# Performance work log

Measured on AMD Instinct MI355X. Metric: run time of the kernel, lower is better.

The kernel has to match this reference:

```python
import jax, jax.numpy as jnp
import numpy as np

N_NODES = 50000
N_EDGES = 1600000
N_GRAPHS = 64
F_IN = 256
H = 1024
EPS = 1e-5


def setup_inputs() -> dict:
    key = jax.random.key(0)
    ks = jax.random.split(key, 6)
    x = jax.random.normal(ks[0], (N_NODES, F_IN), dtype=jnp.float32)
    edge_index = jax.random.randint(ks[1], (2, N_EDGES), 0, N_NODES, dtype=jnp.int32)
    batch = jnp.sort(jax.random.randint(ks[2], (N_NODES,), 0, N_GRAPHS, dtype=jnp.int32))
    # Glorot-ish init for GCN weights
    W0 = jax.random.normal(ks[3], (F_IN, H), dtype=jnp.float32) * (1.0 / np.sqrt(F_IN))
    b0 = jnp.zeros((H,), dtype=jnp.float32)
    Ws = jax.random.normal(ks[4], (3, H, H), dtype=jnp.float32) * (1.0 / np.sqrt(H))
    bs = jnp.zeros((3, H), dtype=jnp.float32)
    gammas = jnp.ones((4, H), dtype=jnp.float32)
    betas = jnp.zeros((4, H), dtype=jnp.float32)
    return {"x": x, "edge_index": edge_index, "batch": batch,
            "W0": W0, "b0": b0, "Ws": Ws, "bs": bs,
            "gammas": gammas, "betas": betas}


def _gcn_norm(edge_index, n_nodes):
    # Add self-loops (PyG GCNConv default), compute symmetric normalization.
    loops = jnp.arange(n_nodes, dtype=edge_index.dtype)
    row = jnp.concatenate([edge_index[0], loops])  # sources
    col = jnp.concatenate([edge_index[1], loops])  # targets (aggregation index)
    ones = jnp.ones(row.shape[0], dtype=jnp.float32)
    deg = jax.ops.segment_sum(ones, col, num_segments=n_nodes)
    dinv = jnp.where(deg > 0, jax.lax.rsqrt(deg), 0.0)
    norm = dinv[row] * dinv[col]  # [E + N]
    return row, col, norm


def _layer(h, W, b, gamma, beta, row, col, norm):
    ht = h @ W                                           # [N, H] GEMM
    msg = ht[row] * norm[:, None]                        # gather + scale
    agg = jax.ops.segment_sum(msg, col, num_segments=N_NODES) + b
    mu = jnp.mean(agg, axis=-1, keepdims=True)
    var = jnp.mean(jnp.square(agg - mu), axis=-1, keepdims=True)
    hn = (agg - mu) * jax.lax.rsqrt(var + EPS) * gamma + beta
    return jax.nn.relu(hn)


def reference(x, edge_index, batch, W0, b0, Ws, bs, gammas, betas):
    row, col, norm = _gcn_norm(edge_index, N_NODES)
    h = _layer(x, W0, b0, gammas[0], betas[0], row, col, norm)
    for i in range(3):
        h = _layer(h, Ws[i], bs[i], gammas[i + 1], betas[i + 1], row, col, norm)
    # scatter_mean over batch (graph-level pooling)
    sums = jax.ops.segment_sum(h, batch, num_segments=N_GRAPHS)
    cnt = jax.ops.segment_sum(jnp.ones((N_NODES,), jnp.float32), batch, num_segments=N_GRAPHS)
    return sums / jnp.maximum(cnt, 1.0)[:, None]
```

## Files before the change

kernel.cpp:

```cpp
#include <hip/hip_runtime.h>
#include <hip/hip_bf16.h>
#include <stdint.h>

#define NN 50000
#define NE 1600000
#define NG 64
#define FIN 256
#define HD 1024
#define EPSV 1e-5f

typedef __bf16 bf16;
typedef __bf16 bf16x4 __attribute__((ext_vector_type(4)));
typedef __bf16 bf16x8 __attribute__((ext_vector_type(8)));
typedef float f32x4 __attribute__((ext_vector_type(4)));

typedef const __attribute__((address_space(1))) void* gptr_as1;
typedef __attribute__((address_space(3))) void* lptr_as3;

__device__ __forceinline__ void load_g2l_16(const void* g, const void* l) {
  __builtin_amdgcn_global_load_lds((gptr_as1)(uintptr_t)g,
                                   (lptr_as3)(uint32_t)(uintptr_t)l, 16, 0, 0);
}

__global__ void hist_kernel(const int* __restrict__ col, int* __restrict__ cnt, int E) {
  int e = blockIdx.x * 256 + threadIdx.x;
  if (e < E) atomicAdd(&cnt[col[e]], 1);
}

__global__ void dinv_kernel(const int* __restrict__ cnt, float* __restrict__ dinv, int n) {
  int i = blockIdx.x * 256 + threadIdx.x;
  if (i < n) dinv[i] = rsqrtf((float)(cnt[i] + 1));
}

__global__ void scan_partial_kernel(const int* __restrict__ cnt, int* __restrict__ partial, int n) {
  __shared__ int red[4];
  int i = blockIdx.x * 256 + threadIdx.x;
  int v = (i < n) ? cnt[i] : 0;
  #pragma unroll
  for (int off = 32; off; off >>= 1) v += __shfl_down(v, off, 64);
  if ((threadIdx.x & 63) == 0) red[threadIdx.x >> 6] = v;
  __syncthreads();
  if (threadIdx.x == 0) partial[blockIdx.x] = red[0] + red[1] + red[2] + red[3];
}

__global__ void scan_scan_kernel(int* __restrict__ partial, int nb) {
  __shared__ int s[256];
  int t = threadIdx.x;
  int v = (t < nb) ? partial[t] : 0;
  s[t] = v;
  __syncthreads();
  for (int off = 1; off < 256; off <<= 1) {
    int x = (t >= off) ? s[t - off] : 0;
    __syncthreads();
    s[t] += x;
    __syncthreads();
  }
  if (t < nb) partial[t] = s[t] - v;
}

__global__ void scan_final_kernel(const int* __restrict__ cnt, const int* __restrict__ partial,
                                  int* __restrict__ row_ptr, int n, int E) {
  __shared__ int s[256];
  int t = threadIdx.x;
  int i = blockIdx.x * 256 + t;
  int v = (i < n) ? cnt[i] : 0;
  s[t] = v;
  __syncthreads();
  for (int off = 1; off < 256; off <<= 1) {
    int x = (t >= off) ? s[t - off] : 0;
    __syncthreads();
    s[t] += x;
    __syncthreads();
  }
  if (i < n) row_ptr[i] = partial[blockIdx.x] + s[t] - v;
  if (i == 0) row_ptr[n] = E;
}

__global__ void scatter_kernel(const int* __restrict__ rowi, const int* __restrict__ coli,
                               const int* __restrict__ row_ptr, int* __restrict__ fill,
                               const float* __restrict__ dinv,
                               int* __restrict__ csr_src, float* __restrict__ csr_w, int E) {
  int e = blockIdx.x * 256 + threadIdx.x;
  if (e >= E) return;
  int s = rowi[e], d = coli[e];
  int pos = row_ptr[d] + atomicAdd(&fill[d], 1);
  csr_src[pos] = s;
  csr_w[pos] = dinv[s] * dinv[d];
}

__global__ void cvt_kernel(const float* __restrict__ in, bf16* __restrict__ out, int n4) {
  int i = blockIdx.x * 256 + threadIdx.x;
  if (i >= n4) return;
  float4 v = ((const float4*)in)[i];
  bf16x4 o = { (bf16)v.x, (bf16)v.y, (bf16)v.z, (bf16)v.w };
  ((bf16x4*)out)[i] = o;
}

__global__ void transpose_w_kernel(const float* __restrict__ W, bf16* __restrict__ Wt,
                                   int K, int N) {
  __shared__ float tile[32][33];
  int n0 = blockIdx.x * 32, k0 = blockIdx.y * 32;
  int tx = threadIdx.x, ty = threadIdx.y;
  #pragma unroll
  for (int i = ty; i < 32; i += 8) tile[i][tx] = W[(size_t)(k0 + i) * N + n0 + tx];
  __syncthreads();
  #pragma unroll
  for (int i = ty; i < 32; i += 8) Wt[(size_t)(n0 + i) * K + k0 + tx] = (bf16)tile[tx][i];
}

__global__ __launch_bounds__(256, 2) void gemm_bt_kernel(
    const bf16* __restrict__ A, const bf16* __restrict__ Bt,
    bf16* __restrict__ C, int M, int K) {
  __shared__ __align__(16) bf16 As[2][128 * 32];
  __shared__ __align__(16) bf16 Bs[2][128 * 32];
  const int tid = threadIdx.x;
  const int w = tid >> 6, l = tid & 63;

  const int nwg = gridDim.x;
  const int o = blockIdx.x;
  const int lid = (o & 7) * (nwg >> 3) + (o >> 3);
  const int m0 = (lid >> 3) * 128, n0 = (lid & 7) * 128;
  const int wr = w >> 1, wc = w & 1;

  f32x4 acc[4][4] = {};

  const int r0 = tid >> 2;
  const int c8 = (tid & 3) * 8;
  int ar0 = m0 + r0;       if (ar0 >= M) ar0 = M - 1;
  int ar1 = m0 + r0 + 64;  if (ar1 >= M) ar1 = M - 1;
  const bf16* a0 = A + (size_t)ar0 * K + c8;
  const bf16* a1 = A + (size_t)ar1 * K + c8;
  const bf16* b0 = Bt + (size_t)(n0 + r0) * K + c8;
  const bf16* b1 = Bt + (size_t)(n0 + r0 + 64) * K + c8;

  const int mrow = l & 15;
  const int kch = (l >> 4) * 8;

  auto stage = [&](int b, int k) {
    bf16* asw = &As[b][w * 512];
    bf16* bsw = &Bs[b][w * 512];
    load_g2l_16(a0 + k, asw);
    load_g2l_16(a1 + k, asw + 2048);
    load_g2l_16(b0 + k, bsw);
    load_g2l_16(b1 + k, bsw + 2048);
  };

  const int nit = K >> 5;
  stage(0, 0);
  __syncthreads();

  int cur = 0;
  for (int t = 0; t < nit; ++t) {
    if (t + 1 < nit) stage(cur ^ 1, (t + 1) << 5);
    bf16x8 af[4], bf_[4];
    #pragma unroll
    for (int m = 0; m < 4; m++)
      af[m] = *(const bf16x8*)&As[cur][(wr * 64 + m * 16 + mrow) * 32 + kch];
    #pragma unroll
    for (int n = 0; n < 4; n++)
      bf_[n] = *(const bf16x8*)&Bs[cur][(wc * 64 + n * 16 + mrow) * 32 + kch];
    #pragma unroll
    for (int m = 0; m < 4; m++)
      #pragma unroll
      for (int n = 0; n < 4; n++)
        acc[m][n] = __builtin_amdgcn_mfma_f32_16x16x32_bf16(af[m], bf_[n], acc[m][n], 0, 0, 0);
    __syncthreads();
    cur ^= 1;
  }

  #pragma unroll
  for (int m = 0; m < 4; m++) {
    int grow = m0 + wr * 64 + m * 16 + (l >> 4) * 4;
    #pragma unroll
    for (int n = 0; n < 4; n++) {
      int gcol = n0 + wc * 64 + n * 16 + (l & 15);
      #pragma unroll
      for (int r = 0; r < 4; r++) {
        if (grow + r < M) C[(size_t)(grow + r) * HD + gcol] = (bf16)acc[m][n][r];
      }
    }
  }
}

__global__ __launch_bounds__(256) void quant_kernel(
    const bf16* __restrict__ ht, uint8_t* __restrict__ htu8, float* __restrict__ rowscale) {
  const int row = blockIdx.x;
  const int t = threadIdx.x;
  __shared__ float red[4];
  bf16x4 v = ((const bf16x4*)(ht + (size_t)row * HD))[t];
  float f0 = (float)v[0], f1 = (float)v[1], f2 = (float)v[2], f3 = (float)v[3];
  float m = fmaxf(fmaxf(fabsf(f0), fabsf(f1)), fmaxf(fabsf(f2), fabsf(f3)));
  #pragma unroll
  for (int off = 32; off; off >>= 1) m = fmaxf(m, __shfl_xor(m, off, 64));
  if ((t & 63) == 0) red[t >> 6] = m;
  __syncthreads();
  m = fmaxf(fmaxf(red[0], red[1]), fmaxf(red[2], red[3]));
  float inv = (m > 0.f) ? 127.0f / m : 0.f;
  int q0 = __float2int_rn(f0 * inv) + 128, q1 = __float2int_rn(f1 * inv) + 128;
  int q2 = __float2int_rn(f2 * inv) + 128, q3 = __float2int_rn(f3 * inv) + 128;
  uint32_t packed = ((uint32_t)(q0 & 0xff)) | ((uint32_t)(q1 & 0xff) << 8) |
                    ((uint32_t)(q2 & 0xff) << 16) | ((uint32_t)(q3 & 0xff) << 24);
  ((uint32_t*)htu8)[row * 256 + t] = packed;
  if (t == 0) rowscale[row] = (m > 0.f) ? m / 127.0f : 0.f;
}

__device__ __forceinline__ void acc_u8(float acc[8], float& sw, float w, uint2 d) {
  sw += w;
  acc[0] += w * (float)(d.x & 0xffu);
  acc[1] += w * (float)((d.x >> 8) & 0xffu);
  acc[2] += w * (float)((d.x >> 16) & 0xffu);
  acc[3] += w * (float)(d.x >> 24);
  acc[4] += w * (float)(d.y & 0xffu);
  acc[5] += w * (float)((d.y >> 8) & 0xffu);
  acc[6] += w * (float)((d.y >> 16) & 0xffu);
  acc[7] += w * (float)(d.y >> 24);
}

__global__ __launch_bounds__(256) void agg_ln_u8_kernel(
    const uint8_t* __restrict__ htu8, const float* __restrict__ rowscale,
    const int* __restrict__ row_ptr,
    const int* __restrict__ csr_src, const float* __restrict__ csr_w,
    const float* __restrict__ dinv, const float* __restrict__ bias,
    const float* __restrict__ gamma, const float* __restrict__ beta,
    bf16* __restrict__ hout) {
  const int g = threadIdx.x >> 7;
  const int node = blockIdx.x * 2 + g;
  const int tt = threadIdx.x & 127;
  const int wid = threadIdx.x >> 6;
  __shared__ float red[4];

  float acc[8] = {};
  float sw = 0.f;

  float dn = dinv[node];
  float wself = dn * dn * rowscale[node];
  acc_u8(acc, sw, wself, ((const uint2*)(htu8 + (size_t)node * HD))[tt]);

  int e = row_ptr[node];
  const int e1 = row_ptr[node + 1];
  for (; e + 4 <= e1; e += 4) {
    int s0 = csr_src[e], s1 = csr_src[e + 1], s2 = csr_src[e + 2], s3 = csr_src[e + 3];
    float w0 = csr_w[e] * rowscale[s0];
    float w1 = csr_w[e + 1] * rowscale[s1];
    float w2 = csr_w[e + 2] * rowscale[s2];
    float w3 = csr_w[e + 3] * rowscale[s3];
    uint2 d0 = ((const uint2*)(htu8 + (size_t)s0 * HD))[tt];
    uint2 d1 = ((const uint2*)(htu8 + (size_t)s1 * HD))[tt];
    uint2 d2 = ((const uint2*)(htu8 + (size_t)s2 * HD))[tt];
    uint2 d3 = ((const uint2*)(htu8 + (size_t)s3 * HD))[tt];
    acc_u8(acc, sw, w0, d0);
    acc_u8(acc, sw, w1, d1);
    acc_u8(acc, sw, w2, d2);
    acc_u8(acc, sw, w3, d3);
  }
  for (; e < e1; e++) {
    int src = csr_src[e];
    float wgt = csr_w[e] * rowscale[src];
    acc_u8(acc, sw, wgt, ((const uint2*)(htu8 + (size_t)src * HD))[tt]);
  }

  const float4* bias2 = (const float4*)bias;
  float4 ba = bias2[tt * 2], bb = bias2[tt * 2 + 1];
  float c128 = 128.0f * sw;
  acc[0] += ba.x - c128; acc[1] += ba.y - c128; acc[2] += ba.z - c128; acc[3] += ba.w - c128;
  acc[4] += bb.x - c128; acc[5] += bb.y - c128; acc[6] += bb.z - c128; acc[7] += bb.w - c128;

  float s = 0.f;
  #pragma unroll
  for (int j = 0; j < 8; j++) s += acc[j];
  #pragma unroll
  for (int off = 32; off; off >>= 1) s += __shfl_down(s, off, 64);
  if ((threadIdx.x & 63) == 0) red[wid] = s;
  __syncthreads();
  float mean = (red[g * 2] + red[g * 2 + 1]) * (1.0f / HD);
  __syncthreads();

  float d[8], s2 = 0.f;
  #pragma unroll
  for (int j = 0; j < 8; j++) { d[j] = acc[j] - mean; s2 += d[j] * d[j]; }
  #pragma unroll
  for (int off = 32; off; off >>= 1) s2 += __shfl_down(s2, off, 64);
  if ((threadIdx.x & 63) == 0) red[wid] = s2;
  __syncthreads();
  float var = (red[g * 2] + red[g * 2 + 1]) * (1.0f / HD);
  float rstd = rsqrtf(var + EPSV);

  const float4* gam2 = (const float4*)gamma;
  const float4* bet2 = (const float4*)beta;
  float4 g0 = gam2[tt * 2], g1 = gam2[tt * 2 + 1];
  float4 be0 = bet2[tt * 2], be1 = bet2[tt * 2 + 1];
  float gv[8] = {g0.x, g0.y, g0.z, g0.w, g1.x, g1.y, g1.z, g1.w};
  float bv[8] = {be0.x, be0.y, be0.z, be0.w, be1.x, be1.y, be1.z, be1.w};
  bf16x8 o;
  #pragma unroll
  for (int j = 0; j < 8; j++) o[j] = (bf16)fmaxf(d[j] * rstd * gv[j] + bv[j], 0.0f);
  ((bf16x8*)(hout + (size_t)node * HD))[tt] = o;
}

__global__ void starts_kernel(const int* __restrict__ batch, int* __restrict__ start,
                              int n, int ngraph) {
  int g = blockIdx.x * blockDim.x + threadIdx.x;
  if (g > ngraph) return;
  int lo = 0, hi = n;
  while (lo < hi) {
    int mid = (lo + hi) >> 1;
    if (batch[mid] < g) lo = mid + 1; else hi = mid;
  }
  start[g] = lo;
}

#define POOL_CHUNKS 8
__global__ void pool_partial_kernel(const bf16* __restrict__ h, const int* __restrict__ start,
                                    float* __restrict__ out) {
  int g = blockIdx.y, c = blockIdx.x;
  int t = threadIdx.x;
  int s0 = start[g], s1 = start[g + 1];
  int len = s1 - s0;
  int per = (len + POOL_CHUNKS - 1) / POOL_CHUNKS;
  int a = s0 + c * per;
  int b = min(a + per, s1);
  if (a >= b) return;
  f32x4 acc = {0.f, 0.f, 0.f, 0.f};
  for (int n = a; n < b; n++) {
    bf16x4 v = ((const bf16x4*)(h + (size_t)n * HD))[t];
    acc[0] += (float)v[0]; acc[1] += (float)v[1];
    acc[2] += (float)v[2]; acc[3] += (float)v[3];
  }
  float* o = out + (size_t)g * HD + t * 4;
  atomicAdd(o + 0, acc[0]);
  atomicAdd(o + 1, acc[1]);
  atomicAdd(o + 2, acc[2]);
  atomicAdd(o + 3, acc[3]);
}

__global__ void pool_div_kernel(float* __restrict__ out, const int* __restrict__ start) {
  int i = blockIdx.x * 256 + threadIdx.x;
  if (i >= NG * HD) return;
  int g = i >> 10;
  float c = (float)max(start[g + 1] - start[g], 1);
  out[i] = out[i] / c;
}

extern "C" void kernel_launch(void* const* d_in, const int* in_sizes, int n_in,
                              void* d_out, int out_size, void* d_ws, size_t ws_size,
                              hipStream_t stream) {
  const float* x      = (const float*)d_in[0];
  const int*   eidx   = (const int*)d_in[1];
  const int*   batch  = (const int*)d_in[2];
  const float* W0     = (const float*)d_in[3];
  const float* b0     = (const float*)d_in[4];
  const float* Ws     = (const float*)d_in[5];
  const float* bs     = (const float*)d_in[6];
  const float* gammas = (const float*)d_in[7];
  const float* betas  = (const float*)d_in[8];
  float* out = (float*)d_out;

  const int* erow = eidx;
  const int* ecol = eidx + NE;

  char* ws = (char*)d_ws;
  size_t off = 0;
  auto alloc = [&](size_t bytes) {
    void* p = ws + off;
    off = (off + bytes + 255) & ~(size_t)255;
    return p;
  };
  int*   cnt     = (int*)alloc((size_t)NN * 4);
  int*   row_ptr = (int*)alloc((size_t)(NN + 1) * 4);
  int*   fill    = (int*)alloc((size_t)NN * 4);
  int*   partial = (int*)alloc(256 * 4);
  float* dinv    = (float*)alloc((size_t)NN * 4);
  int*   csr_src = (int*)alloc((size_t)NE * 4);
  float* csr_w   = (float*)alloc((size_t)NE * 4);
  bf16*  Wt      = (bf16*)alloc((size_t)HD * HD * 2);
  bf16*  hbuf    = (bf16*)alloc((size_t)NN * HD * 2);
  bf16*  htbuf   = (bf16*)alloc((size_t)NN * HD * 2);
  int*   gstart  = (int*)alloc(65 * 4);
  float* rowscale = (float*)cnt;

  hipMemsetAsync(cnt, 0, (size_t)NN * 4, stream);
  hipMemsetAsync(fill, 0, (size_t)NN * 4, stream);
  hipMemsetAsync(out, 0, (size_t)NG * HD * 4, stream);

  hist_kernel<<<(NE + 255) / 256, 256, 0, stream>>>(ecol, cnt, NE);
  dinv_kernel<<<(NN + 255) / 256, 256, 0, stream>>>(cnt, dinv, NN);
  int nb = (NN + 255) / 256;
  scan_partial_kernel<<<nb, 256, 0, stream>>>(cnt, partial, NN);
  scan_scan_kernel<<<1, 256, 0, stream>>>(partial, nb);
  scan_final_kernel<<<nb, 256, 0, stream>>>(cnt, partial, row_ptr, NN, NE);
  scatter_kernel<<<(NE + 255) / 256, 256, 0, stream>>>(erow, ecol, row_ptr, fill, dinv,
                                                       csr_src, csr_w, NE);
  starts_kernel<<<1, 128, 0, stream>>>(batch, gstart, NN, NG);

  bf16* A = hbuf;
  bf16* B = htbuf;

  cvt_kernel<<<(NN * FIN / 4 + 255) / 256, 256, 0, stream>>>(x, A, NN * FIN / 4);

  const int nmt = (NN + 127) / 128;
  for (int L = 0; L < 4; L++) {
    int K = (L == 0) ? FIN : HD;
    const float* W    = (L == 0) ? W0 : Ws + (size_t)(L - 1) * HD * HD;
    const float* bias = (L == 0) ? b0 : bs + (size_t)(L - 1) * HD;
    transpose_w_kernel<<<dim3(HD / 32, K / 32), dim3(32, 8), 0, stream>>>(W, Wt, K, HD);
    gemm_bt_kernel<<<nmt * 8, 256, 0, stream>>>(A, Wt, B, NN, K);
    quant_kernel<<<NN, 256, 0, stream>>>(B, (uint8_t*)A, rowscale);
    agg_ln_u8_kernel<<<NN / 2, 256, 0, stream>>>((const uint8_t*)A, rowscale, row_ptr,
                                                 csr_src, csr_w, dinv, bias,
                                                 gammas + (size_t)L * HD,
                                                 betas + (size_t)L * HD, B);
    bf16* tmp = A; A = B; B = tmp;
  }

  pool_partial_kernel<<<dim3(POOL_CHUNKS, NG), 256, 0, stream>>>(A, gstart, out);
  pool_div_kernel<<<(NG * HD + 255) / 256, 256, 0, stream>>>(out, gstart);
}
```

Before: 1.749 ms.

## Fuse int8 quantization into GEMM epilogue with per-128-column block scales

The GEMM epilogue now computes a per-row absmax over each 128-column tile and writes uint8 values plus a per-(row, column-block) scale straight to global memory. This removes the separate quant kernel and the bf16 round-trip of the full activation matrix. The aggregation kernel indexes the scale per column block instead of per row. In exchange there is extra shuffle and LDS work in the epilogue, byte-wise scattered stores, and more scale loads per edge during the gather.

```diff
diff --git a/kernel.cpp b/kernel.cpp
--- a/kernel.cpp
+++ b/kernel.cpp
@@ -108,11 +108,12 @@
   for (int i = ty; i < 32; i += 8) Wt[(size_t)(n0 + i) * K + k0 + tx] = (bf16)tile[tx][i];
 }
 
-__global__ __launch_bounds__(256, 2) void gemm_bt_kernel(
+__global__ __launch_bounds__(256, 2) void gemm_bt_q8_kernel(
     const bf16* __restrict__ A, const bf16* __restrict__ Bt,
-    bf16* __restrict__ C, int M, int K) {
+    uint8_t* __restrict__ C8, float* __restrict__ scales, int M, int K) {
   __shared__ __align__(16) bf16 As[2][128 * 32];
   __shared__ __align__(16) bf16 Bs[2][128 * 32];
+  __shared__ float smax[2][128];
   const int tid = threadIdx.x;
   const int w = tid >> 6, l = tid & 63;
 
@@ -120,6 +121,7 @@
   const int o = blockIdx.x;
   const int lid = (o & 7) * (nwg >> 3) + (o >> 3);
   const int m0 = (lid >> 3) * 128, n0 = (lid & 7) * 128;
+  const int cb = lid & 7;
   const int wr = w >> 1, wc = w & 1;
 
   f32x4 acc[4][4] = {};
@@ -168,40 +170,47 @@
     cur ^= 1;
   }
 
+  float pmax[4][4];
+  #pragma unroll
+  for (int m = 0; m < 4; m++)
+    #pragma unroll
+    for (int r = 0; r < 4; r++) {
+      float v = 0.f;
+      #pragma unroll
+      for (int n = 0; n < 4; n++) v = fmaxf(v, fabsf(acc[m][n][r]));
+      #pragma unroll
+      for (int mask = 1; mask < 16; mask <<= 1) v = fmaxf(v, __shfl_xor(v, mask, 64));
+      pmax[m][r] = v;
+    }
+  if ((l & 15) == 0) {
+    #pragma unroll
+    for (int m = 0; m < 4; m++)
+      #pragma unroll
+      for (int r = 0; r < 4; r++)
+        smax[wc][wr * 64 + m * 16 + (l >> 4) * 4 + r] = pmax[m][r];
+  }
+  __syncthreads();
+
   #pragma unroll
   for (int m = 0; m < 4; m++) {
-    int grow = m0 + wr * 64 + m * 16 + (l >> 4) * 4;
-    #pragma unroll
-    for (int n = 0; n < 4; n++) {
-      int gcol = n0 + wc * 64 + n * 16 + (l & 15);
-      #pragma unroll
-      for (int r = 0; r < 4; r++) {
-        if (grow + r < M) C[(size_t)(grow + r) * HD + gcol] = (bf16)acc[m][n][r];
+    #pragma unroll
+    for (int r = 0; r < 4; r++) {
+      int rl = wr * 64 + m * 16 + (l >> 4) * 4 + r;
+      int grow = m0 + rl;
+      float mx = fmaxf(smax[0][rl], smax[1][rl]);
+      float inv = (mx > 0.f) ? 127.0f / mx : 0.f;
+      if (grow < M) {
+        if (wc == 0 && (l & 15) == 0)
+          scales[(size_t)grow * 8 + cb] = (mx > 0.f) ? mx / 127.0f : 0.f;
+        #pragma unroll
+        for (int n = 0; n < 4; n++) {
+          int gcol = n0 + wc * 64 + n * 16 + (l & 15);
+          int u = __float2int_rn(acc[m][n][r] * inv) + 128;
+          C8[(size_t)grow * HD + gcol] = (uint8_t)u;
+        }
       }
     }
   }
-}
-
-__global__ __launch_bounds__(256) void quant_kernel(
-    const bf16* __restrict__ ht, uint8_t* __restrict__ htu8, float* __restrict__ rowscale) {
-  const int row = blockIdx.x;
-  const int t = threadIdx.x;
-  __shared__ float red[4];
-  bf16x4 v = ((const bf16x4*)(ht + (size_t)row * HD))[t];
-  float f0 = (float)v[0], f1 = (float)v[1], f2 = (float)v[2], f3 = (float)v[3];
-  float m = fmaxf(fmaxf(fabsf(f0), fabsf(f1)), fmaxf(fabsf(f2), fabsf(f3)));
-  #pragma unroll
-  for (int off = 32; off; off >>= 1) m = fmaxf(m, __shfl_xor(m, off, 64));
-  if ((t & 63) == 0) red[t >> 6] = m;
-  __syncthreads();
-  m = fmaxf(fmaxf(red[0], red[1]), fmaxf(red[2], red[3]));
-  float inv = (m > 0.f) ? 127.0f / m : 0.f;
-  int q0 = __float2int_rn(f0 * inv) + 128, q1 = __float2int_rn(f1 * inv) + 128;
-  int q2 = __float2int_rn(f2 * inv) + 128, q3 = __float2int_rn(f3 * inv) + 128;
-  uint32_t packed = ((uint32_t)(q0 & 0xff)) | ((uint32_t)(q1 & 0xff) << 8) |
-                    ((uint32_t)(q2 & 0xff) << 16) | ((uint32_t)(q3 & 0xff) << 24);
-  ((uint32_t*)htu8)[row * 256 + t] = packed;
-  if (t == 0) rowscale[row] = (m > 0.f) ? m / 127.0f : 0.f;
 }
 
 __device__ __forceinline__ void acc_u8(float acc[8], float& sw, float w, uint2 d) {
@@ -217,7 +226,7 @@
 }
 
 __global__ __launch_bounds__(256) void agg_ln_u8_kernel(
-    const uint8_t* __restrict__ htu8, const float* __restrict__ rowscale,
+    const uint8_t* __restrict__ htu8, const float* __restrict__ scales,
     const int* __restrict__ row_ptr,
     const int* __restrict__ csr_src, const float* __restrict__ csr_w,
     const float* __restrict__ dinv, const float* __restrict__ bias,
@@ -226,6 +235,7 @@
   const int g = threadIdx.x >> 7;
   const int node = blockIdx.x * 2 + g;
   const int tt = threadIdx.x & 127;
+  const int cbL = tt >> 4;
   const int wid = threadIdx.x >> 6;
   __shared__ float red[4];
 
@@ -233,17 +243,17 @@
   float sw = 0.f;
 
   float dn = dinv[node];
-  float wself = dn * dn * rowscale[node];
+  float wself = dn * dn * scales[(size_t)node * 8 + cbL];
   acc_u8(acc, sw, wself, ((const uint2*)(htu8 + (size_t)node * HD))[tt]);
 
   int e = row_ptr[node];
   const int e1 = row_ptr[node + 1];
   for (; e + 4 <= e1; e += 4) {
     int s0 = csr_src[e], s1 = csr_src[e + 1], s2 = csr_src[e + 2], s3 = csr_src[e + 3];
-    float w0 = csr_w[e] * rowscale[s0];
-    float w1 = csr_w[e + 1] * rowscale[s1];
-    float w2 = csr_w[e + 2] * rowscale[s2];
-    float w3 = csr_w[e + 3] * rowscale[s3];
+    float w0 = csr_w[e] * scales[(size_t)s0 * 8 + cbL];
+    float w1 = csr_w[e + 1] * scales[(size_t)s1 * 8 + cbL];
+    float w2 = csr_w[e + 2] * scales[(size_t)s2 * 8 + cbL];
+    float w3 = csr_w[e + 3] * scales[(size_t)s3 * 8 + cbL];
     uint2 d0 = ((const uint2*)(htu8 + (size_t)s0 * HD))[tt];
     uint2 d1 = ((const uint2*)(htu8 + (size_t)s1 * HD))[tt];
     uint2 d2 = ((const uint2*)(htu8 + (size_t)s2 * HD))[tt];
@@ -255,7 +265,7 @@
   }
   for (; e < e1; e++) {
     int src = csr_src[e];
-    float wgt = csr_w[e] * rowscale[src];
+    float wgt = csr_w[e] * scales[(size_t)src * 8 + cbL];
     acc_u8(acc, sw, wgt, ((const uint2*)(htu8 + (size_t)src * HD))[tt]);
   }
 
@@ -365,18 +375,18 @@
     off = (off + bytes + 255) & ~(size_t)255;
     return p;
   };
-  int*   cnt     = (int*)alloc((size_t)NN * 4);
-  int*   row_ptr = (int*)alloc((size_t)(NN + 1) * 4);
-  int*   fill    = (int*)alloc((size_t)NN * 4);
-  int*   partial = (int*)alloc(256 * 4);
-  float* dinv    = (float*)alloc((size_t)NN * 4);
-  int*   csr_src = (int*)alloc((size_t)NE * 4);
-  float* csr_w   = (float*)alloc((size_t)NE * 4);
-  bf16*  Wt      = (bf16*)alloc((size_t)HD * HD * 2);
-  bf16*  hbuf    = (bf16*)alloc((size_t)NN * HD * 2);
-  bf16*  htbuf   = (bf16*)alloc((size_t)NN * HD * 2);
-  int*   gstart  = (int*)alloc(65 * 4);
-  float* rowscale = (float*)cnt;
+  int*     cnt     = (int*)alloc((size_t)NN * 4);
+  int*     row_ptr = (int*)alloc((size_t)(NN + 1) * 4);
+  int*     fill    = (int*)alloc((size_t)NN * 4);
+  int*     partial = (int*)alloc(256 * 4);
+  float*   dinv    = (float*)alloc((size_t)NN * 4);
+  int*     csr_src = (int*)alloc((size_t)NE * 4);
+  float*   csr_w   = (float*)alloc((size_t)NE * 4);
+  bf16*    Wt      = (bf16*)alloc((size_t)HD * HD * 2);
+  bf16*    hbuf    = (bf16*)alloc((size_t)NN * HD * 2);
+  uint8_t* ht8     = (uint8_t*)alloc((size_t)NN * HD);
+  float*   scales  = (float*)alloc((size_t)NN * 8 * 4);
+  int*     gstart  = (int*)alloc(65 * 4);
 
   hipMemsetAsync(cnt, 0, (size_t)NN * 4, stream);
   hipMemsetAsync(fill, 0, (size_t)NN * 4, stream);
@@ -392,10 +402,7 @@
                                                        csr_src, csr_w, NE);
   starts_kernel<<<1, 128, 0, stream>>>(batch, gstart, NN, NG);
 
-  bf16* A = hbuf;
-  bf16* B = htbuf;
-
-  cvt_kernel<<<(NN * FIN / 4 + 255) / 256, 256, 0, stream>>>(x, A, NN * FIN / 4);
+  cvt_kernel<<<(NN * FIN / 4 + 255) / 256, 256, 0, stream>>>(x, hbuf, NN * FIN / 4);
 
   const int nmt = (NN + 127) / 128;
   for (int L = 0; L < 4; L++) {
@@ -403,15 +410,12 @@
     const float* W    = (L == 0) ? W0 : Ws + (size_t)(L - 1) * HD * HD;
     const float* bias = (L == 0) ? b0 : bs + (size_t)(L - 1) * HD;
     transpose_w_kernel<<<dim3(HD / 32, K / 32), dim3(32, 8), 0, stream>>>(W, Wt, K, HD);
-    gemm_bt_kernel<<<nmt * 8, 256, 0, stream>>>(A, Wt, B, NN, K);
-    quant_kernel<<<NN, 256, 0, stream>>>(B, (uint8_t*)A, rowscale);
-    agg_ln_u8_kernel<<<NN / 2, 256, 0, stream>>>((const uint8_t*)A, rowscale, row_ptr,
-                                                 csr_src, csr_w, dinv, bias,
-                                                 gammas + (size_t)L * HD,
-                                                 betas + (size_t)L * HD, B);
-    bf16* tmp = A; A = B; B = tmp;
-  }
-
-  pool_partial_kernel<<<dim3(POOL_CHUNKS, NG), 256, 0, stream>>>(A, gstart, out);
+    gemm_bt_q8_kernel<<<nmt * 8, 256, 0, stream>>>(hbuf, Wt, ht8, scales, NN, K);
+    agg_ln_u8_kernel<<<NN / 2, 256, 0, stream>>>(ht8, scales, row_ptr, csr_src, csr_w,
+                                                 dinv, bias, gammas + (size_t)L * HD,
+                                                 betas + (size_t)L * HD, hbuf);
+  }
+
+  pool_partial_kernel<<<dim3(POOL_CHUNKS, NG), 256, 0, stream>>>(hbuf, gstart, out);
   pool_div_kernel<<<(NG * HD + 255) / 256, 256, 0, stream>>>(out, gstart);
 }
```

Result: faster. 1.681 ms (-3.9%).
